# Optimization experiments

Hardware: AMD Instinct MI355X
Metric: run time of the kernel (lower is better)

Reference implementation:

```python
import jax, jax.numpy as jnp
import numpy as np

N_NODES = 20000
N_EDGES = 320000
B, F_IN, H_DIM, P = 4, 16, 64, 12


def _glorot(key, shape):
    fan_in, fan_out = shape[0], shape[-1]
    lim = float(np.sqrt(6.0 / (fan_in + fan_out)))
    return jax.random.uniform(key, shape, jnp.float32, -lim, lim)


def setup_inputs() -> dict:
    key = jax.random.key(0)
    ks = jax.random.split(key, 20)
    x = jax.random.normal(ks[0], (B, N_NODES, F_IN, P), jnp.float32)
    edge_index = jax.random.randint(ks[1], (2, N_EDGES), 0, N_NODES, jnp.int64)
    edge_weight = jax.random.uniform(ks[2], (N_EDGES,), jnp.float32)
    # GCNConv weights (in, out) and biases for z/r/h gates
    Wg_z = _glorot(ks[3], (F_IN, H_DIM)); bg_z = jnp.zeros((H_DIM,), jnp.float32)
    Wg_r = _glorot(ks[4], (F_IN, H_DIM)); bg_r = jnp.zeros((H_DIM,), jnp.float32)
    Wg_h = _glorot(ks[5], (F_IN, H_DIM)); bg_h = jnp.zeros((H_DIM,), jnp.float32)
    # Linear layers on concat([conv_out, H]) -> (2H, H)
    Wl_z = _glorot(ks[6], (2 * H_DIM, H_DIM)); bl_z = jax.random.uniform(ks[7], (H_DIM,), jnp.float32, -0.1, 0.1)
    Wl_r = _glorot(ks[8], (2 * H_DIM, H_DIM)); bl_r = jax.random.uniform(ks[9], (H_DIM,), jnp.float32, -0.1, 0.1)
    Wl_h = _glorot(ks[10], (2 * H_DIM, H_DIM)); bl_h = jax.random.uniform(ks[11], (H_DIM,), jnp.float32, -0.1, 0.1)
    att = jax.random.uniform(ks[12], (P,), jnp.float32)  # attention logits over periods
    W_out = _glorot(ks[13], (H_DIM, P)); b_out = jax.random.uniform(ks[14], (P,), jnp.float32, -0.1, 0.1)
    return {"x": x, "edge_index": edge_index, "edge_weight": edge_weight,
            "Wg_z": Wg_z, "bg_z": bg_z, "Wg_r": Wg_r, "bg_r": bg_r, "Wg_h": Wg_h, "bg_h": bg_h,
            "Wl_z": Wl_z, "bl_z": bl_z, "Wl_r": Wl_r, "bl_r": bl_r, "Wl_h": Wl_h, "bl_h": bl_h,
            "att": att, "W_out": W_out, "b_out": b_out}


def reference(x, edge_index, edge_weight, Wg_z, bg_z, Wg_r, bg_r, Wg_h, bg_h,
              Wl_z, bl_z, Wl_r, bl_r, Wl_h, bl_h, att, W_out, b_out):
    Bsz, N, F, Pn = x.shape
    Hh = Wg_z.shape[1]
    # --- gcn_norm: add self loops (weight 1.0), D^-1/2 (A+I) D^-1/2 ---
    loop = jnp.arange(N)
    src = jnp.concatenate([edge_index[0], loop])
    dst = jnp.concatenate([edge_index[1], loop])
    w = jnp.concatenate([edge_weight, jnp.ones((N,), x.dtype)])
    deg = jnp.zeros((N,), x.dtype).at[dst].add(w)
    dinv = jnp.where(deg > 0, jax.lax.rsqrt(deg), 0.0)
    norm = dinv[src] * w * dinv[dst]  # (E+N,)
    # --- propagate raw features once for all periods: (A_hat X) W == A_hat (X W) ---
    xf = x.reshape(Bsz, N, F * Pn)
    msg = xf[:, src, :] * norm[None, :, None]            # (B, E+N, F*P) gather
    agg = jnp.zeros((Bsz, N, F * Pn), x.dtype).at[:, dst, :].add(msg)  # scatter-add
    agg = agg.reshape(Bsz, N, F, Pn)
    # --- A3TGCN2: per-period single GRU step from H=0, attention-pooled ---
    probs = jax.nn.softmax(att)
    H0 = jnp.zeros((Bsz, N, Hh), x.dtype)

    def step(acc, inp):
        a, p = inp  # a: (B, N, F) aggregated features of this period
        cz = a @ Wg_z + bg_z
        cr = a @ Wg_r + bg_r
        ch = a @ Wg_h + bg_h
        Z = jax.nn.sigmoid(jnp.concatenate([cz, H0], -1) @ Wl_z + bl_z)
        R = jax.nn.sigmoid(jnp.concatenate([cr, H0], -1) @ Wl_r + bl_r)
        Ht = jnp.tanh(jnp.concatenate([ch, H0 * R], -1) @ Wl_h + bl_h)
        Hn = Z * H0 + (1.0 - Z) * Ht
        return acc + p * Hn, None

    a_seq = jnp.moveaxis(agg, -1, 0)  # (P, B, N, F)
    Hacc, _ = jax.lax.scan(step, H0, (a_seq, probs))
    # --- trailing ReLU + Linear ---
    return jax.nn.relu(Hacc) @ W_out + b_out  # (B, N, P)
```

## Files before the change

kernel.cpp:

```cpp
#include <hip/hip_runtime.h>
#include <cstdint>
#include <cstddef>

#define NN 20000
#define NE 320000
#define NB 4
#define NF 16
#define NH 64
#define NP 12
#define FP (NF*NP)
#define ROWB (FP*2)
#define NROWB (NB*ROWB)
#define GRIDA 5000

typedef _Float16 h2_t __attribute__((ext_vector_type(2)));
typedef _Float16 h4_t __attribute__((ext_vector_type(4)));
typedef float    f4_t __attribute__((ext_vector_type(4)));

union U32H2 { unsigned u; h2_t h; };
union U64H4 { uint2 u; h4_t h; };

__global__ __launch_bounds__(256) void k_pre1(const float* __restrict__ x,
                                              _Float16* __restrict__ xh,
                                              const int* __restrict__ ei,
                                              const float* __restrict__ ew,
                                              float* deg, int* counts) {
    int blk = blockIdx.x;
    if (blk < 3750) {
        int i = blk * 256 + threadIdx.x;
        int n = i / 48;
        int c = i - n * 48;
        const float4* xf = (const float4*)x;
        h4_t* xo = (h4_t*)xh;
#pragma unroll
        for (int b = 0; b < NB; ++b) {
            float4 v = xf[(size_t)b * (NN * 48) + i];
            h4_t o = { (_Float16)v.x, (_Float16)v.y, (_Float16)v.z, (_Float16)v.w };
            xo[(n * NB + b) * 48 + c] = o;
        }
    } else {
        int e = (blk - 3750) * 256 + threadIdx.x;
        int dst = ei[NE + e];
        atomicAdd(&deg[dst], ew[e]);
        atomicAdd(&counts[dst], 1);
    }
}

__global__ __launch_bounds__(1024) void k_prep(
        const float* __restrict__ deg, float* __restrict__ dinv,
        const int* __restrict__ counts, int* __restrict__ offsets, int* gbase,
        const float* __restrict__ Wg_z, const float* __restrict__ bg_z,
        const float* __restrict__ Wg_h, const float* __restrict__ bg_h,
        const float* __restrict__ Wl_z, const float* __restrict__ bl_z,
        const float* __restrict__ Wl_h, const float* __restrict__ bl_h,
        const float* __restrict__ att, const float* __restrict__ W_out,
        uint2* __restrict__ wfrag, uint2* __restrict__ wofrag,
        float* bz_eff, float* bh_eff, float* probs) {
    int blk = blockIdx.x;
    int t = threadIdx.x;
    if (blk < 20) {
        __shared__ int sums[1024];
        __shared__ int base_sh;
        int i = blk * 1000 + t;
        int slots = 0;
        if (t < 1000) {
            dinv[i] = rsqrtf(1.0f + deg[i]);
            slots = counts[i] + 1;
        }
        sums[t] = slots;
        __syncthreads();
        for (int off = 1; off < 1024; off <<= 1) {
            int v = (t >= off) ? sums[t - off] : 0;
            __syncthreads();
            sums[t] += v;
            __syncthreads();
        }
        if (t == 1023) base_sh = atomicAdd(gbase, sums[1023]);
        __syncthreads();
        if (t < 1000) offsets[i] = base_sh + sums[t] - slots;
        return;
    }
    __shared__ float wzl[NF][NH + 1];
    __shared__ float whl[NF][NH + 1];
    {
        int f = t >> 6, j = t & 63;
        float sz = 0.f, sh = 0.f;
        for (int k = 0; k < NH; ++k) {
            sz += Wg_z[f * NH + k] * Wl_z[k * NH + j];
            sh += Wg_h[f * NH + k] * Wl_h[k * NH + j];
        }
        wzl[f][j] = sz;
        whl[f][j] = sh;
    }
    if (t < NH) {
        float bz = bl_z[t], bh = bl_h[t];
        for (int k = 0; k < NH; ++k) {
            bz += bg_z[k] * Wl_z[k * NH + t];
            bh += bg_h[k] * Wl_h[k * NH + t];
        }
        bz_eff[t] = bz;
        bh_eff[t] = bh;
    }
    if (t == 0) {
        float m = att[0];
        for (int p = 1; p < NP; ++p) m = fmaxf(m, att[p]);
        float s = 0.f, e_[NP];
        for (int p = 0; p < NP; ++p) { e_[p] = expf(att[p] - m); s += e_[p]; }
        for (int p = 0; p < 16; ++p) probs[p] = (p < NP) ? e_[p] / s : 0.f;
    }
    __syncthreads();
    if (t < 512) {
        int ln = t & 63, c = (t >> 6) & 3, zh = t >> 8;
        int kb = 4 * (ln >> 4);
        int j  = 16 * c + (ln & 15);
        float v0, v1, v2, v3;
        if (zh == 0) { v0 = wzl[kb][j]; v1 = wzl[kb+1][j]; v2 = wzl[kb+2][j]; v3 = wzl[kb+3][j]; }
        else         { v0 = whl[kb][j]; v1 = whl[kb+1][j]; v2 = whl[kb+2][j]; v3 = whl[kb+3][j]; }
        union { _Float16 h[4]; uint2 u; } pk;
        pk.h[0] = (_Float16)v0; pk.h[1] = (_Float16)v1;
        pk.h[2] = (_Float16)v2; pk.h[3] = (_Float16)v3;
        wfrag[(zh * 4 + c) * 64 + ln] = pk.u;
    }
    if (t < 256) {
        int ln = t & 63, s = t >> 6;
        int kj = 16 * s + 4 * (ln >> 4);
        int nn_ = ln & 15;
        union { _Float16 h[4]; uint2 u; } pk;
        for (int i = 0; i < 4; ++i)
            pk.h[i] = (_Float16)((nn_ < NP) ? W_out[(kj + i) * NP + nn_] : 0.f);
        wofrag[s * 64 + ln] = pk.u;
    }
}

__global__ __launch_bounds__(256) void k_fill(const int* __restrict__ ei,
                                              const float* __restrict__ ew,
                                              const float* __restrict__ dinv,
                                              const int* __restrict__ offsets,
                                              const int* __restrict__ counts,
                                              int* cursor, uint2* __restrict__ erec) {
    int e = blockIdx.x * 256 + threadIdx.x;
    if (e < NE) {
        int s = ei[e];
        int d = ei[NE + e];
        float nm = dinv[s] * ew[e] * dinv[d];
        int pos = atomicAdd(&cursor[d], 1);
        int idx = offsets[d] + pos;
        _Float16 hn = (_Float16)nm;
        U32H2 w; w.h = (h2_t){hn, hn};
        erec[idx] = make_uint2((unsigned)(s * NROWB), w.u);
    } else if (e < NE + NN) {
        int node = e - NE;
        float di = dinv[node];
        _Float16 hn = (_Float16)(di * di);
        U32H2 w; w.h = (h2_t){hn, hn};
        erec[offsets[node] + counts[node]] = make_uint2((unsigned)(node * NROWB), w.u);
    }
}

__global__ __launch_bounds__(256) void k_main(
        const _Float16* __restrict__ xh,
        const int* __restrict__ offsets, const int* __restrict__ counts,
        const uint2* __restrict__ erec, const uint2* __restrict__ wfrag,
        const float* __restrict__ bz_eff, const float* __restrict__ bh_eff,
        const float* __restrict__ probs, _Float16* __restrict__ rout) {
    __shared__ unsigned a_lds[2][NB][96];
    __shared__ uint2    wz_lds[512];
    __shared__ float    bzh_lds[128];
    __shared__ float    pr_lds[16];

    int t = threadIdx.x;
    wz_lds[t]       = wfrag[t];
    wz_lds[t + 256] = wfrag[t + 256];
    if (t < 128) bzh_lds[t] = (t < 64) ? bz_eff[t] : bh_eff[t - 64];
    if (t < 16)  pr_lds[t] = probs[t];
    __syncthreads();

    int wv = t >> 6;
    int lane = t & 63;
    int half = lane >> 5;
    int g = lane >> 4, p = lane & 15;
    int pe = (p < NP) ? p : 0;
    int q = pe >> 1, hs = pe & 1;

    const char* xbase = (const char*)xh;
    int lb = wv * ROWB + (lane & 31) * 12;

    for (int k = 0, it = 0; k < 4; ++k, ++it) {
        int n = blockIdx.x + k * GRIDA;
        int beg = offsets[n];
        int last = beg + counts[n];
        int end = last + 1;

        h2_t A0 = {(_Float16)0.f, (_Float16)0.f};
        h2_t A1 = A0, A2 = A0;

        uint2 qa0, qa1, qa2, qa3, qa4, qa5, qa6, qa7;
        {
            int e0 = beg;
#define LQ(K, QV) { int s_ = e0 + 2*(K) + half; int i_ = s_ < last ? s_ : last; QV = erec[i_]; }
            LQ(0,qa0) LQ(1,qa1) LQ(2,qa2) LQ(3,qa3) LQ(4,qa4) LQ(5,qa5) LQ(6,qa6) LQ(7,qa7)
#undef LQ
        }

        int ecur = beg;
        while (true) {
            int enext = ecur + 16;
            bool more = enext < end;
            uint2 qb0, qb1, qb2, qb3, qb4, qb5, qb6, qb7;
            if (more) {
#define LQ(K, QV) { int s_ = enext + 2*(K) + half; int i_ = s_ < last ? s_ : last; QV = erec[i_]; }
                LQ(0,qb0) LQ(1,qb1) LQ(2,qb2) LQ(3,qb3) LQ(4,qb4) LQ(5,qb5) LQ(6,qb6) LQ(7,qb7)
#undef LQ
            }
            uint3 u0 = *(const uint3*)(xbase + qa0.x + lb);
            uint3 u1 = *(const uint3*)(xbase + qa1.x + lb);
            uint3 u2 = *(const uint3*)(xbase + qa2.x + lb);
            uint3 u3 = *(const uint3*)(xbase + qa3.x + lb);
            uint3 u4 = *(const uint3*)(xbase + qa4.x + lb);
            uint3 u5 = *(const uint3*)(xbase + qa5.x + lb);
            uint3 u6 = *(const uint3*)(xbase + qa6.x + lb);
            uint3 u7 = *(const uint3*)(xbase + qa7.x + lb);
#define ACC(K, QV, UV) { \
                int s_ = ecur + 2*(K) + half; \
                unsigned w_ = (s_ <= last) ? QV.y : 0u; \
                U32H2 wu; wu.u = w_; \
                U32H2 x0; x0.u = UV.x; U32H2 x1; x1.u = UV.y; U32H2 x2; x2.u = UV.z; \
                A0 += wu.h * x0.h; A1 += wu.h * x1.h; A2 += wu.h * x2.h; }
            ACC(0,qa0,u0) ACC(1,qa1,u1) ACC(2,qa2,u2) ACC(3,qa3,u3)
            ACC(4,qa4,u4) ACC(5,qa5,u5) ACC(6,qa6,u6) ACC(7,qa7,u7)
#undef ACC
            if (!more) break;
            qa0=qb0; qa1=qb1; qa2=qb2; qa3=qb3; qa4=qb4; qa5=qb5; qa6=qb6; qa7=qb7;
            ecur = enext;
        }

        {
            U32H2 t0, t1, t2, s0, s1, s2;
            t0.h = A0; t1.h = A1; t2.h = A2;
            s0.u = (unsigned)__shfl_xor((int)t0.u, 32, 64);
            s1.u = (unsigned)__shfl_xor((int)t1.u, 32, 64);
            s2.u = (unsigned)__shfl_xor((int)t2.u, 32, 64);
            A0 += s0.h; A1 += s1.h; A2 += s2.h;
        }

        if (lane < 32) {
            unsigned* aw = &a_lds[it & 1][wv][0];
            U32H2 t0, t1, t2; t0.h = A0; t1.h = A1; t2.h = A2;
            int L = lane;
            aw[3 * L + 0] = t0.u;
            aw[3 * L + 1] = t1.u;
            aw[3 * L + 2] = t2.u;
        }

        const unsigned* abw = &a_lds[it & 1][wv][24 * g + q];
        U32H2 w0; w0.u = abw[0];
        U32H2 w1; w1.u = abw[6];
        U32H2 w2; w2.u = abw[12];
        U32H2 w3; w3.u = abw[18];
        h4_t A = { w0.h[hs], w1.h[hs], w2.h[hs], w3.h[hs] };

        f4_t accz[4], acch[4];
#pragma unroll
        for (int c = 0; c < 4; ++c) {
            float bzv = bzh_lds[16 * c + p];
            float bhv = bzh_lds[64 + 16 * c + p];
            accz[c] = (f4_t){bzv, bzv, bzv, bzv};
            acch[c] = (f4_t){bhv, bhv, bhv, bhv};
        }
#pragma unroll
        for (int c = 0; c < 4; ++c) {
            U64H4 fz; fz.u = wz_lds[c * 64 + lane];
            U64H4 fh; fh.u = wz_lds[(4 + c) * 64 + lane];
            accz[c] = __builtin_amdgcn_mfma_f32_16x16x16f16(A, fz.h, accz[c], 0, 0, 0);
            acch[c] = __builtin_amdgcn_mfma_f32_16x16x16f16(A, fh.h, acch[c], 0, 0, 0);
        }

        float rh0, rh1, rh2, rh3;
#pragma unroll
        for (int c = 0; c < 4; ++c) {
            float partial = 0.f;
#pragma unroll
            for (int r = 0; r < 4; ++r) {
                float zz = accz[c][r];
                float hh = acch[c][r];
                float sn = __builtin_amdgcn_rcpf(1.f + __expf(zz));
                float th = 1.f - 2.f * __builtin_amdgcn_rcpf(__expf(2.f * hh) + 1.f);
                partial = fmaf(pr_lds[4 * g + r], sn * th, partial);
            }
            partial += __shfl_xor(partial, 16, 64);
            partial += __shfl_xor(partial, 32, 64);
            float v = fmaxf(partial, 0.f);
            if (c == 0) rh0 = v; else if (c == 1) rh1 = v; else if (c == 2) rh2 = v; else rh3 = v;
        }
        float r01 = (g & 1) ? rh1 : rh0;
        float r23 = (g & 1) ? rh3 : rh2;
        float rsel = (g & 2) ? r23 : r01;
        rout[((size_t)wv * NN + n) * NH + lane] = (_Float16)rsel;
    }
}

__global__ __launch_bounds__(256) void k_out(
        const _Float16* __restrict__ rout, const uint2* __restrict__ wofrag,
        const float* __restrict__ b_out, float* __restrict__ out) {
    int lane = threadIdx.x & 63;
    int g = lane >> 4, p = lane & 15;
    int tile = blockIdx.x * 4 + (threadIdx.x >> 6);
    int u0 = tile * 16;

    float bo = b_out[p < NP ? p : 0];
    f4_t co = (f4_t){bo, bo, bo, bo};
    const h4_t* arow = (const h4_t*)(rout + (size_t)(u0 + p) * NH);
#pragma unroll
    for (int s = 0; s < 4; ++s) {
        h4_t Ao = arow[4 * s + g];
        U64H4 Bo; Bo.u = wofrag[s * 64 + lane];
        co = __builtin_amdgcn_mfma_f32_16x16x16f16(Ao, Bo.h, co, 0, 0, 0);
    }
    if (p < NP) {
#pragma unroll
        for (int r = 0; r < 4; ++r)
            out[(size_t)(u0 + 4 * g + r) * NP + p] = co[r];
    }
}


extern "C" void kernel_launch(void* const* d_in, const int* in_sizes, int n_in,
                              void* d_out, int out_size, void* d_ws, size_t ws_size,
                              hipStream_t stream) {
    const float* x     = (const float*)d_in[0];
    const int*   ei    = (const int*)d_in[1];
    const float* ew    = (const float*)d_in[2];
    const float* Wg_z  = (const float*)d_in[3];
    const float* bg_z  = (const float*)d_in[4];
    const float* Wg_h  = (const float*)d_in[7];
    const float* bg_h  = (const float*)d_in[8];
    const float* Wl_z  = (const float*)d_in[9];
    const float* bl_z  = (const float*)d_in[10];
    const float* Wl_h  = (const float*)d_in[13];
    const float* bl_h  = (const float*)d_in[14];
    const float* att   = (const float*)d_in[15];
    const float* W_out = (const float*)d_in[16];
    const float* b_out = (const float*)d_in[17];
    float*       out   = (float*)d_out;

    char* p = (char*)d_ws;
    auto alloc = [&](size_t bytes) -> void* {
        void* r = (void*)p;
        p += (bytes + 255) & ~(size_t)255;
        return r;
    };
    const size_t PAD_NN = ((size_t)NN * 4 + 255) & ~(size_t)255;
    float*     deg     = (float*)alloc(NN * 4);
    int*       counts  = (int*)  alloc(NN * 4);
    int*       cursor  = (int*)  alloc(NN * 4);
    int*       gbase   = (int*)  alloc(256);
    float*     dinv    = (float*)alloc(NN * 4);
    int*       offsets = (int*)  alloc(NN * 4);
    uint2*     erec    = (uint2*)alloc((size_t)(NE + NN) * 8);
    uint2*     wfrag   = (uint2*)alloc(512 * 8);
    uint2*     wofrag  = (uint2*)alloc(256 * 8);
    float*     bz_eff  = (float*)alloc(NH * 4);
    float*     bh_eff  = (float*)alloc(NH * 4);
    float*     probs   = (float*)alloc(16 * 4);
    _Float16*  xh      = (_Float16*)alloc((size_t)NN * NROWB);
    _Float16*  rout    = (_Float16*)alloc((size_t)NN * NB * NH * 2);

    hipMemsetAsync(deg, 0, PAD_NN * 3 + 256, stream);

    k_pre1 <<<5000, 256, 0, stream>>>(x, xh, ei, ew, deg, counts);
    k_prep <<<21, 1024, 0, stream>>>(deg, dinv, counts, offsets, gbase,
                                     Wg_z, bg_z, Wg_h, bg_h, Wl_z, bl_z, Wl_h, bl_h,
                                     att, W_out, wfrag, wofrag, bz_eff, bh_eff, probs);
    k_fill <<<(NE + NN + 255) / 256, 256, 0, stream>>>(ei, ew, dinv, offsets, counts, cursor, erec);
    k_main <<<GRIDA, 256, 0, stream>>>(xh, offsets, counts, erec, wfrag,
                                       bz_eff, bh_eff, probs, rout);
    k_out  <<<1250, 256, 0, stream>>>(rout, wofrag, b_out, out);
}
```

Baseline: 183.0 us.

## Split fused gather+GRU kernel into separate gather and GRU kernels

The fused k_main kernel is split into k_gather, which does the sparse neighbor aggregation and writes the aggregated fp16 features to a new intermediate buffer, and k_gru, which reads that buffer and runs the gate matmuls and activations. The aim is to let each phase run with its own register and LDS footprint and occupancy, so the latency-bound gather is not held back by the GRU's shared memory and registers. In exchange it adds a global round trip of the NN*NB*192 fp16 aggregate buffer and one more kernel launch.

```diff
diff --git a/kernel.cpp b/kernel.cpp
--- a/kernel.cpp
+++ b/kernel.cpp
@@ -12,6 +12,7 @@
 #define ROWB (FP*2)
 #define NROWB (NB*ROWB)
 #define GRIDA 5000
+#define GRIDG 2500
 
 typedef _Float16 h2_t __attribute__((ext_vector_type(2)));
 typedef _Float16 h4_t __attribute__((ext_vector_type(4)));
@@ -157,35 +158,21 @@
     }
 }
 
-__global__ __launch_bounds__(256) void k_main(
+__global__ __launch_bounds__(256) void k_gather(
         const _Float16* __restrict__ xh,
         const int* __restrict__ offsets, const int* __restrict__ counts,
-        const uint2* __restrict__ erec, const uint2* __restrict__ wfrag,
-        const float* __restrict__ bz_eff, const float* __restrict__ bh_eff,
-        const float* __restrict__ probs, _Float16* __restrict__ rout) {
-    __shared__ unsigned a_lds[2][NB][96];
-    __shared__ uint2    wz_lds[512];
-    __shared__ float    bzh_lds[128];
-    __shared__ float    pr_lds[16];
-
+        const uint2* __restrict__ erec, _Float16* __restrict__ aout) {
     int t = threadIdx.x;
-    wz_lds[t]       = wfrag[t];
-    wz_lds[t + 256] = wfrag[t + 256];
-    if (t < 128) bzh_lds[t] = (t < 64) ? bz_eff[t] : bh_eff[t - 64];
-    if (t < 16)  pr_lds[t] = probs[t];
-    __syncthreads();
-
     int wv = t >> 6;
     int lane = t & 63;
     int half = lane >> 5;
-    int g = lane >> 4, p = lane & 15;
-    int pe = (p < NP) ? p : 0;
-    int q = pe >> 1, hs = pe & 1;
+    int L = lane & 31;
+    int lb0 = L * 12;
 
     const char* xbase = (const char*)xh;
-    int lb = wv * ROWB + (lane & 31) * 12;
-
-    for (int k = 0, it = 0; k < 4; ++k, ++it) {
+    int lb = wv * ROWB + lb0;
+
+    for (int k = 0; k < 4; ++k) {
         int n = blockIdx.x + k * GRIDA;
         int beg = offsets[n];
         int last = beg + counts[n];
@@ -234,22 +221,57 @@
             ecur = enext;
         }
 
-        {
-            U32H2 t0, t1, t2, s0, s1, s2;
-            t0.h = A0; t1.h = A1; t2.h = A2;
-            s0.u = (unsigned)__shfl_xor((int)t0.u, 32, 64);
-            s1.u = (unsigned)__shfl_xor((int)t1.u, 32, 64);
-            s2.u = (unsigned)__shfl_xor((int)t2.u, 32, 64);
-            A0 += s0.h; A1 += s1.h; A2 += s2.h;
-        }
+        U32H2 t0, t1, t2, s0, s1, s2;
+        t0.h = A0; t1.h = A1; t2.h = A2;
+        s0.u = (unsigned)__shfl_xor((int)t0.u, 32, 64);
+        s1.u = (unsigned)__shfl_xor((int)t1.u, 32, 64);
+        s2.u = (unsigned)__shfl_xor((int)t2.u, 32, 64);
+        t0.h += s0.h; t1.h += s1.h; t2.h += s2.h;
+
+        if (lane < 32) {
+            uint3 w3; w3.x = t0.u; w3.y = t1.u; w3.z = t2.u;
+            *(uint3*)((char*)aout + ((size_t)wv * NN + n) * ROWB + lb0) = w3;
+        }
+    }
+}
+
+__global__ __launch_bounds__(256) void k_gru(
+        const _Float16* __restrict__ aout, const uint2* __restrict__ wfrag,
+        const float* __restrict__ bz_eff, const float* __restrict__ bh_eff,
+        const float* __restrict__ probs, _Float16* __restrict__ rout) {
+    __shared__ unsigned a_lds[2][NB][96];
+    __shared__ uint2    wz_lds[512];
+    __shared__ float    bzh_lds[128];
+    __shared__ float    pr_lds[16];
+
+    int t = threadIdx.x;
+    wz_lds[t]       = wfrag[t];
+    wz_lds[t + 256] = wfrag[t + 256];
+    if (t < 128) bzh_lds[t] = (t < 64) ? bz_eff[t] : bh_eff[t - 64];
+    if (t < 16)  pr_lds[t] = probs[t];
+    __syncthreads();
+
+    int wv = t >> 6;
+    int lane = t & 63;
+    int L = lane & 31;
+    int g = lane >> 4, p = lane & 15;
+    int pe = (p < NP) ? p : 0;
+    int q = pe >> 1, hs = pe & 1;
+
+    const char* abase = (const char*)aout;
+    int wav = blockIdx.x * 4 + wv;
+
+    for (int k = 0, it = 0; k < 8; ++k, ++it) {
+        int u = wav + k * 10000;
+
+        uint3 av = make_uint3(0u, 0u, 0u);
+        if (lane < 32) av = *(const uint3*)(abase + (size_t)u * ROWB + L * 12);
 
         if (lane < 32) {
             unsigned* aw = &a_lds[it & 1][wv][0];
-            U32H2 t0, t1, t2; t0.h = A0; t1.h = A1; t2.h = A2;
-            int L = lane;
-            aw[3 * L + 0] = t0.u;
-            aw[3 * L + 1] = t1.u;
-            aw[3 * L + 2] = t2.u;
+            aw[3 * L + 0] = av.x;
+            aw[3 * L + 1] = av.y;
+            aw[3 * L + 2] = av.z;
         }
 
         const unsigned* abw = &a_lds[it & 1][wv][24 * g + q];
@@ -295,7 +317,7 @@
         float r01 = (g & 1) ? rh1 : rh0;
         float r23 = (g & 1) ? rh3 : rh2;
         float rsel = (g & 2) ? r23 : r01;
-        rout[((size_t)wv * NN + n) * NH + lane] = (_Float16)rsel;
+        rout[(size_t)u * NH + lane] = (_Float16)rsel;
     }
 }
 
@@ -363,16 +385,17 @@
     float*     bh_eff  = (float*)alloc(NH * 4);
     float*     probs   = (float*)alloc(16 * 4);
     _Float16*  xh      = (_Float16*)alloc((size_t)NN * NROWB);
+    _Float16*  aout    = (_Float16*)alloc((size_t)NN * NROWB);
     _Float16*  rout    = (_Float16*)alloc((size_t)NN * NB * NH * 2);
 
     hipMemsetAsync(deg, 0, PAD_NN * 3 + 256, stream);
 
-    k_pre1 <<<5000, 256, 0, stream>>>(x, xh, ei, ew, deg, counts);
-    k_prep <<<21, 1024, 0, stream>>>(deg, dinv, counts, offsets, gbase,
-                                     Wg_z, bg_z, Wg_h, bg_h, Wl_z, bl_z, Wl_h, bl_h,
-                                     att, W_out, wfrag, wofrag, bz_eff, bh_eff, probs);
-    k_fill <<<(NE + NN + 255) / 256, 256, 0, stream>>>(ei, ew, dinv, offsets, counts, cursor, erec);
-    k_main <<<GRIDA, 256, 0, stream>>>(xh, offsets, counts, erec, wfrag,
-                                       bz_eff, bh_eff, probs, rout);
-    k_out  <<<1250, 256, 0, stream>>>(rout, wofrag, b_out, out);
-}
+    k_pre1   <<<5000, 256, 0, stream>>>(x, xh, ei, ew, deg, counts);
+    k_prep   <<<21, 1024, 0, stream>>>(deg, dinv, counts, offsets, gbase,
+                                       Wg_z, bg_z, Wg_h, bg_h, Wl_z, bl_z, Wl_h, bl_h,
+                                       att, W_out, wfrag, wofrag, bz_eff, bh_eff, probs);
+    k_fill   <<<(NE + NN + 255) / 256, 256, 0, stream>>>(ei, ew, dinv, offsets, counts, cursor, erec);
+    k_gather <<<GRIDA, 256, 0, stream>>>(xh, offsets, counts, erec, aout);
+    k_gru    <<<GRIDG, 256, 0, stream>>>(aout, wfrag, bz_eff, bh_eff, probs, rout);
+    k_out    <<<1250, 256, 0, stream>>>(rout, wofrag, b_out, out);
+}
```

Result: slower. 209.9 us (+14.7%).
